# Performance work log

Measured on AMD Instinct MI355X. Metric: run time of the kernel, lower is better.

## Reference

```python
import jax, jax.numpy as jnp
import numpy as np

N_NODES = 100000
N_EDGES = 1600000
DIM = 128
N_LAYERS = 3
N_GRAPHS = 2048


def setup_inputs() -> dict:
    key = jax.random.key(0)
    ks = jax.random.split(key, 6)
    x = jax.random.normal(ks[0], (N_NODES, DIM), dtype=jnp.float32)
    edge_index = jax.random.randint(ks[1], (2, N_EDGES), 0, N_NODES, dtype=jnp.int64)
    batch = jnp.sort(jax.random.randint(ks[2], (N_NODES,), 0, N_GRAPHS, dtype=jnp.int64))
    scale = 1.0 / np.sqrt(DIM)
    W1 = jax.random.normal(ks[3], (N_LAYERS, DIM, DIM), dtype=jnp.float32) * scale
    b1 = jnp.zeros((N_LAYERS, DIM), dtype=jnp.float32)
    W2 = jax.random.normal(ks[4], (N_LAYERS, DIM, DIM), dtype=jnp.float32) * scale
    b2 = jnp.zeros((N_LAYERS, DIM), dtype=jnp.float32)
    return {"x": x, "edge_index": edge_index, "batch": batch,
            "W1": W1, "b1": b1, "W2": W2, "b2": b2}


def reference(x, edge_index, batch, W1, b1, W2, b2):
    src, dst = edge_index[0], edge_index[1]
    n = x.shape[0]
    n_layers = W1.shape[0]
    for l in range(n_layers):
        # GINConv (eps=0): h_i = MLP( sum_{j in N(i)} x_j + x_i )
        agg = jax.ops.segment_sum(x[src], dst, num_segments=n)  # [N, D]
        h = agg + x
        h = jnp.maximum(h @ W1[l] + b1[l], 0.0) @ W2[l] + b2[l]
        x = jnp.maximum(h, 0.0)  # outer self.act
    # global_mean_pool over graph ids
    sums = jax.ops.segment_sum(x, batch, num_segments=N_GRAPHS)  # [G, D]
    counts = jax.ops.segment_sum(jnp.ones((n,), x.dtype), batch, num_segments=N_GRAPHS)
    return sums / jnp.maximum(counts, 1.0)[:, None]
```

## Files before the change

kernel.cpp:

```cpp
#include <hip/hip_runtime.h>
#include <hip/hip_bf16.h>
#include <stdint.h>

#define N_NODES  100000
#define N_PAD    100032
#define N_EDGES  1600000
#define DIM      128
#define N_LAYERS 3
#define N_GRAPHS 2048

#define BSHIFT   9
#define NBUCKET  196
#define P1CHUNK  8192
#define P1GRID   196

typedef _Float16 f16;
typedef __attribute__((ext_vector_type(2))) _Float16 f16x2;
typedef __attribute__((ext_vector_type(4))) _Float16 f16x4;
typedef __attribute__((ext_vector_type(8))) _Float16 f16x8;
typedef __attribute__((ext_vector_type(4))) float f32x4;

#define MFMA16(a, b, c) __builtin_amdgcn_mfma_f32_16x16x32_f16((a), (b), (c), 0, 0, 0)

#define OFF_OFFS  0u
#define OFF_BHT   400064u
#define OFF_BST   400896u
#define OFF_GCUR  401728u
#define OFF_BLKH  402560u
#define OFF_ESRC  556288u
#define OFF_PAIR  6956288u
#define OFF_X16   19756288u
#define OFF_A16   45364480u
#define OFF_B16   70972672u
#define OFF_W1T   96580864u
#define OFF_W2T   96679168u


__global__ __launch_bounds__(256) void k_bhist(const int* __restrict__ dst,
                                               int* __restrict__ btot, int* __restrict__ blkh) {
    __shared__ int h[NBUCKET];
    int tid = threadIdx.x, b = blockIdx.x;
    if (tid < NBUCKET) h[tid] = 0;
    __syncthreads();
    int base = b * P1CHUNK;
    int n = min(P1CHUNK, N_EDGES - base);
    for (int i = tid; i < n; i += 256)
        atomicAdd(&h[dst[base + i] >> BSHIFT], 1);
    __syncthreads();
    if (tid < NBUCKET) {
        blkh[b * NBUCKET + tid] = h[tid];
        atomicAdd(&btot[tid], h[tid]);
    }
}

__global__ void k_bscan(const int* __restrict__ btot, int* __restrict__ bstart,
                        int* __restrict__ gcursor, int* __restrict__ offs) {
    __shared__ int s[NBUCKET + 1];
    if (threadIdx.x == 0) {
        int run = 0;
        for (int i = 0; i < NBUCKET; i++) { s[i] = run; run += btot[i]; }
        s[NBUCKET] = run;
    }
    __syncthreads();
    int t = threadIdx.x;
    if (t <= NBUCKET) bstart[t] = s[t];
    if (t < NBUCKET)  gcursor[t] = s[t];
    if (t == 0) offs[N_NODES] = N_EDGES;
}

__global__ __launch_bounds__(256) void k_part1(const int* __restrict__ src, const int* __restrict__ dst,
                                               const int* __restrict__ blkh, int* __restrict__ gcursor,
                                               uint2* __restrict__ pairs) {
    __shared__ int gbase[NBUCKET];
    __shared__ int cur[NBUCKET];
    int tid = threadIdx.x, b = blockIdx.x;
    if (tid < NBUCKET) {
        int h = blkh[b * NBUCKET + tid];
        gbase[tid] = atomicAdd(&gcursor[tid], h);
        cur[tid] = 0;
    }
    __syncthreads();
    int base = b * P1CHUNK;
    int n = min(P1CHUNK, N_EDGES - base);
    for (int i = tid; i < n; i += 256) {
        int d = dst[base + i], s = src[base + i];
        int bin = d >> BSHIFT;
        int slot = atomicAdd(&cur[bin], 1);
        uint2 p; p.x = (unsigned)d; p.y = (unsigned)s;
        pairs[gbase[bin] + slot] = p;
    }
}

__global__ __launch_bounds__(256) void k_part2(const uint2* __restrict__ pairs,
                                               const int* __restrict__ bstart,
                                               int* __restrict__ offs, int* __restrict__ esrc) {
    __shared__ int cnt[512];
    __shared__ int excl[512];
    __shared__ int sc[256];
    int t = threadIdx.x, b = blockIdx.x;
    int n0 = b << BSHIFT;
    int nn = min(512, N_NODES - n0);
    int e0 = bstart[b], e1 = bstart[b + 1];
    cnt[t] = 0; cnt[t + 256] = 0;
    __syncthreads();
    for (int i = e0 + t; i < e1; i += 256)
        atomicAdd(&cnt[pairs[i].x & 511], 1);
    __syncthreads();
    int a = cnt[2 * t], psum = a + cnt[2 * t + 1];
    sc[t] = psum;
    __syncthreads();
    for (int off = 1; off < 256; off <<= 1) {
        int v = (t >= off) ? sc[t - off] : 0;
        __syncthreads();
        sc[t] += v;
        __syncthreads();
    }
    int pairExcl = sc[t] - psum;
    excl[2 * t] = pairExcl;
    excl[2 * t + 1] = pairExcl + a;
    __syncthreads();
    for (int j = t; j < nn; j += 256) offs[n0 + j] = e0 + excl[j];
    __syncthreads();
    for (int i = e0 + t; i < e1; i += 256) {
        uint2 p = pairs[i];
        int pos = e0 + atomicAdd(&excl[p.x & 511], 1);
        esrc[pos] = (int)p.y;
    }
}


__global__ void k_cvtX(const float* __restrict__ x, f16* __restrict__ o) {
    size_t i = ((size_t)blockIdx.x * 256 + threadIdx.x) * 8;
    float4 v0 = *(const float4*)&x[i];
    float4 v1 = *(const float4*)&x[i + 4];
    f16x8 h;
    h[0] = (f16)v0.x; h[1] = (f16)v0.y; h[2] = (f16)v0.z; h[3] = (f16)v0.w;
    h[4] = (f16)v1.x; h[5] = (f16)v1.y; h[6] = (f16)v1.z; h[7] = (f16)v1.w;
    *(f16x8*)&o[i] = h;
}

__global__ void k_cvtW(const float* __restrict__ W, f16* __restrict__ Wt) {
    int t = blockIdx.x * 256 + threadIdx.x;
    int l = t >> 14;
    int kn = t & 16383;
    int k = kn >> 7, n = kn & 127;
    Wt[l * 16384 + n * 128 + k] = (f16)W[t];
}


#define BM 64
#define LDS_K 136

__global__ __launch_bounds__(256, 4) void k_fused(
    const f16* __restrict__ xin, f16* __restrict__ xout,
    const int* __restrict__ offs, const int* __restrict__ esrc,
    const f16* __restrict__ W1t, const float* __restrict__ b1,
    const f16* __restrict__ W2t, const float* __restrict__ b2)
{
    __shared__ __align__(16) f16 tile[BM * LDS_K];
    int tid  = threadIdx.x;
    int lane = tid & 63;
    int w    = tid >> 6;
    int fr   = lane & 15;
    int fg   = lane >> 4;
    int row0 = blockIdx.x * BM;

    {
        int g = fg, c = fr;
        const f16x8* xr = (const f16x8*)xin;
        int srcLane = g << 4;
#pragma unroll
        for (int s_ = 0; s_ < 4; s_++) {
            int node = row0 + w * 16 + s_ * 4 + g;
            float acc[8];
            if (node < N_NODES) {
                int e0 = offs[node], e1 = offs[node + 1];
                f16x8 sv = xr[(size_t)node * 16 + c];
#pragma unroll
                for (int j = 0; j < 8; j++) acc[j] = (float)sv[j];
                for (int base = e0; base < e1; base += 16) {
                    int ncur = e1 - base; if (ncur > 16) ncur = 16;
                    int ev = esrc[base + (c < ncur ? c : ncur - 1)];
                    int k = 0;
                    for (; k + 4 <= ncur; k += 4) {
                        int s0 = __shfl(ev, srcLane + k);
                        int s1 = __shfl(ev, srcLane + k + 1);
                        int s2 = __shfl(ev, srcLane + k + 2);
                        int s3 = __shfl(ev, srcLane + k + 3);
                        f16x8 v0 = xr[(size_t)s0 * 16 + c];
                        f16x8 v1 = xr[(size_t)s1 * 16 + c];
                        f16x8 v2 = xr[(size_t)s2 * 16 + c];
                        f16x8 v3 = xr[(size_t)s3 * 16 + c];
#pragma unroll
                        for (int j = 0; j < 8; j++)
                            acc[j] += (float)v0[j] + (float)v1[j] + (float)v2[j] + (float)v3[j];
                    }
                    for (; k < ncur; k++) {
                        int s = __shfl(ev, srcLane + k);
                        f16x8 v = xr[(size_t)s * 16 + c];
#pragma unroll
                        for (int j = 0; j < 8; j++) acc[j] += (float)v[j];
                    }
                }
            } else {
#pragma unroll
                for (int j = 0; j < 8; j++) acc[j] = 0.f;
            }
            int r = w * 16 + s_ * 4 + g;
            f16x8 o;
#pragma unroll
            for (int j = 0; j < 8; j++) o[j] = (f16)acc[j];
            *(f16x8*)&tile[r * LDS_K + c * 8] = o;
        }
    }
    __syncthreads();

    f16x8 wf[2][4];
    float4 bv[2];
#pragma unroll
    for (int nt = 0; nt < 2; nt++) {
        int col = w * 32 + nt * 16 + fr;
#pragma unroll
        for (int ks = 0; ks < 4; ks++)
            wf[nt][ks] = *(const f16x8*)&W1t[col * DIM + ks * 32 + fg * 8];
        bv[nt] = *(const float4*)&b1[w * 32 + nt * 16 + fg * 4];
    }

    f32x4 acc[4][2];
#pragma unroll
    for (int mt = 0; mt < 4; mt++)
#pragma unroll
        for (int nt = 0; nt < 2; nt++) acc[mt][nt] = (f32x4){0.f, 0.f, 0.f, 0.f};

#pragma unroll
    for (int mt = 0; mt < 4; mt++)
#pragma unroll
        for (int ks = 0; ks < 4; ks++) {
            f16x8 a = *(const f16x8*)&tile[(mt * 16 + fr) * LDS_K + ks * 32 + fg * 8];
            acc[mt][0] = MFMA16(wf[0][ks], a, acc[mt][0]);
            acc[mt][1] = MFMA16(wf[1][ks], a, acc[mt][1]);
        }
    __syncthreads();

#pragma unroll
    for (int mt = 0; mt < 4; mt++)
#pragma unroll
        for (int nt = 0; nt < 2; nt++) {
            f16x4 hv;
            hv[0] = (f16)fmaxf(acc[mt][nt][0] + bv[nt].x, 0.f);
            hv[1] = (f16)fmaxf(acc[mt][nt][1] + bv[nt].y, 0.f);
            hv[2] = (f16)fmaxf(acc[mt][nt][2] + bv[nt].z, 0.f);
            hv[3] = (f16)fmaxf(acc[mt][nt][3] + bv[nt].w, 0.f);
            *(f16x4*)&tile[(mt * 16 + fr) * LDS_K + w * 32 + nt * 16 + fg * 4] = hv;
        }

#pragma unroll
    for (int nt = 0; nt < 2; nt++) {
        int col = w * 32 + nt * 16 + fr;
#pragma unroll
        for (int ks = 0; ks < 4; ks++)
            wf[nt][ks] = *(const f16x8*)&W2t[col * DIM + ks * 32 + fg * 8];
        bv[nt] = *(const float4*)&b2[w * 32 + nt * 16 + fg * 4];
    }
    __syncthreads();

#pragma unroll
    for (int mt = 0; mt < 4; mt++)
#pragma unroll
        for (int nt = 0; nt < 2; nt++) acc[mt][nt] = (f32x4){0.f, 0.f, 0.f, 0.f};

#pragma unroll
    for (int mt = 0; mt < 4; mt++)
#pragma unroll
        for (int ks = 0; ks < 4; ks++) {
            f16x8 a = *(const f16x8*)&tile[(mt * 16 + fr) * LDS_K + ks * 32 + fg * 8];
            acc[mt][0] = MFMA16(wf[0][ks], a, acc[mt][0]);
            acc[mt][1] = MFMA16(wf[1][ks], a, acc[mt][1]);
        }

#pragma unroll
    for (int mt = 0; mt < 4; mt++)
#pragma unroll
        for (int nt = 0; nt < 2; nt++) {
            f16x4 ov;
            ov[0] = (f16)fmaxf(acc[mt][nt][0] + bv[nt].x, 0.f);
            ov[1] = (f16)fmaxf(acc[mt][nt][1] + bv[nt].y, 0.f);
            ov[2] = (f16)fmaxf(acc[mt][nt][2] + bv[nt].z, 0.f);
            ov[3] = (f16)fmaxf(acc[mt][nt][3] + bv[nt].w, 0.f);
            *(f16x4*)&xout[(size_t)(row0 + mt * 16 + fr) * DIM + w * 32 + nt * 16 + fg * 4] = ov;
        }
}


__global__ void k_pool(const f16* __restrict__ xf, const int* __restrict__ batch,
                       float* __restrict__ out) {
    int g = blockIdx.x;
    int d = threadIdx.x;
    int lo = 0, hi = N_NODES;
    while (lo < hi) { int m = (lo + hi) >> 1; if (batch[m] < g) lo = m + 1; else hi = m; }
    int start = lo;
    hi = N_NODES;
    while (lo < hi) { int m = (lo + hi) >> 1; if (batch[m] <= g) lo = m + 1; else hi = m; }
    int end = lo;
    float acc = 0.f;
    for (int i = start; i < end; i++) acc += (float)xf[(size_t)i * DIM + d];
    float cntf = (float)(end - start);
    out[(size_t)g * DIM + d] = acc / fmaxf(cntf, 1.f);
}


extern "C" void kernel_launch(void* const* d_in, const int* in_sizes, int n_in,
                              void* d_out, int out_size, void* d_ws, size_t ws_size,
                              hipStream_t stream) {
    const float* x     = (const float*)d_in[0];
    const int*   ei    = (const int*)d_in[1];
    const int*   batch = (const int*)d_in[2];
    const float* W1    = (const float*)d_in[3];
    const float* b1    = (const float*)d_in[4];
    const float* W2    = (const float*)d_in[5];
    const float* b2    = (const float*)d_in[6];
    const int* src = ei;
    const int* dst = ei + N_EDGES;

    char* ws = (char*)d_ws;
    int*   offs  = (int*)(ws + OFF_OFFS);
    int*   btot  = (int*)(ws + OFF_BHT);
    int*   bst   = (int*)(ws + OFF_BST);
    int*   gcur  = (int*)(ws + OFF_GCUR);
    int*   blkh  = (int*)(ws + OFF_BLKH);
    int*   esrc  = (int*)(ws + OFF_ESRC);
    uint2* pairs = (uint2*)(ws + OFF_PAIR);
    f16*   x16   = (f16*)(ws + OFF_X16);
    f16*   a16   = (f16*)(ws + OFF_A16);
    f16*   b16   = (f16*)(ws + OFF_B16);
    f16*   w1t   = (f16*)(ws + OFF_W1T);
    f16*   w2t   = (f16*)(ws + OFF_W2T);
    float* outp  = (float*)d_out;

    hipMemsetAsync(btot, 0, NBUCKET * sizeof(int), stream);
    k_bhist<<<P1GRID, 256, 0, stream>>>(dst, btot, blkh);
    k_bscan<<<1, 256, 0, stream>>>(btot, bst, gcur, offs);
    k_part1<<<P1GRID, 256, 0, stream>>>(src, dst, blkh, gcur, pairs);
    k_part2<<<NBUCKET, 256, 0, stream>>>(pairs, bst, offs, esrc);

    k_cvtX<<<6250, 256, 0, stream>>>(x, x16);
    k_cvtW<<<192, 256, 0, stream>>>(W1, w1t);
    k_cvtW<<<192, 256, 0, stream>>>(W2, w2t);

    const f16* xin = x16;
    for (int l = 0; l < N_LAYERS; ++l) {
        f16* xoutb = (l == 1) ? b16 : a16;
        k_fused<<<N_PAD / BM, 256, 0, stream>>>(xin, xoutb, offs, esrc,
                                                w1t + (size_t)l * DIM * DIM, b1 + (size_t)l * DIM,
                                                w2t + (size_t)l * DIM * DIM, b2 + (size_t)l * DIM);
        xin = xoutb;
    }

    k_pool<<<N_GRAPHS, 128, 0, stream>>>(xin, batch, outp);
}
```

Measured before the change: 349.8 us.

## Pack CSR partition pairs into 32-bit and restructure neighbor gather per node

The bucket size for the CSR build is halved so each bucket holds 256 destination nodes. This lets each (src, dst) pair be packed into a single 32-bit word (src in the high bits, local dst in the low 8 bits), halving the traffic of the partition pass. The fused layer kernel now has each wavefront process one node at a time, with its four 16-lane groups striding through the edges. It combines the partial sums with cross-lane xor shuffles, replacing the per-group node assignment and the shuffles that broadcast edge indices. The occupancy hint in the launch bounds is also dropped. The new gather works on 16 nodes per wave sequentially and adds a reduction step per node, which may expose more latency.

```diff
diff --git a/kernel.cpp b/kernel.cpp
--- a/kernel.cpp
+++ b/kernel.cpp
@@ -9,10 +9,10 @@
 #define N_LAYERS 3
 #define N_GRAPHS 2048
 
-#define BSHIFT   9
-#define NBUCKET  196
-#define P1CHUNK  8192
-#define P1GRID   196
+#define BSHIFT   8
+#define NBUCKET  391
+#define P1CHUNK  4096
+#define P1GRID   391
 
 typedef _Float16 f16;
 typedef __attribute__((ext_vector_type(2))) _Float16 f16x2;
@@ -24,32 +24,32 @@
 
 #define OFF_OFFS  0u
 #define OFF_BHT   400064u
-#define OFF_BST   400896u
-#define OFF_GCUR  401728u
-#define OFF_BLKH  402560u
-#define OFF_ESRC  556288u
-#define OFF_PAIR  6956288u
-#define OFF_X16   19756288u
-#define OFF_A16   45364480u
-#define OFF_B16   70972672u
-#define OFF_W1T   96580864u
-#define OFF_W2T   96679168u
+#define OFF_BST   401664u
+#define OFF_GCUR  403264u
+#define OFF_BLKH  404864u
+#define OFF_ESRC  1016448u
+#define OFF_PAIR  7416448u
+#define OFF_X16   13816448u
+#define OFF_A16   39424640u
+#define OFF_B16   65032832u
+#define OFF_W1T   90641024u
+#define OFF_W2T   90739328u
 
 
 __global__ __launch_bounds__(256) void k_bhist(const int* __restrict__ dst,
                                                int* __restrict__ btot, int* __restrict__ blkh) {
     __shared__ int h[NBUCKET];
     int tid = threadIdx.x, b = blockIdx.x;
-    if (tid < NBUCKET) h[tid] = 0;
+    for (int i = tid; i < NBUCKET; i += 256) h[i] = 0;
     __syncthreads();
     int base = b * P1CHUNK;
     int n = min(P1CHUNK, N_EDGES - base);
     for (int i = tid; i < n; i += 256)
         atomicAdd(&h[dst[base + i] >> BSHIFT], 1);
     __syncthreads();
-    if (tid < NBUCKET) {
-        blkh[b * NBUCKET + tid] = h[tid];
-        atomicAdd(&btot[tid], h[tid]);
+    for (int i = tid; i < NBUCKET; i += 256) {
+        blkh[b * NBUCKET + i] = h[i];
+        atomicAdd(&btot[i], h[i]);
     }
 }
 
@@ -63,21 +63,21 @@
     }
     __syncthreads();
     int t = threadIdx.x;
-    if (t <= NBUCKET) bstart[t] = s[t];
-    if (t < NBUCKET)  gcursor[t] = s[t];
+    for (int i = t; i <= NBUCKET; i += 256) bstart[i] = s[i];
+    for (int i = t; i < NBUCKET; i += 256)  gcursor[i] = s[i];
     if (t == 0) offs[N_NODES] = N_EDGES;
 }
 
 __global__ __launch_bounds__(256) void k_part1(const int* __restrict__ src, const int* __restrict__ dst,
                                                const int* __restrict__ blkh, int* __restrict__ gcursor,
-                                               uint2* __restrict__ pairs) {
+                                               uint32_t* __restrict__ pairs) {
     __shared__ int gbase[NBUCKET];
     __shared__ int cur[NBUCKET];
     int tid = threadIdx.x, b = blockIdx.x;
-    if (tid < NBUCKET) {
-        int h = blkh[b * NBUCKET + tid];
-        gbase[tid] = atomicAdd(&gcursor[tid], h);
-        cur[tid] = 0;
+    for (int i = tid; i < NBUCKET; i += 256) {
+        int h = blkh[b * NBUCKET + i];
+        gbase[i] = atomicAdd(&gcursor[i], h);
+        cur[i] = 0;
     }
     __syncthreads();
     int base = b * P1CHUNK;
@@ -86,28 +86,27 @@
         int d = dst[base + i], s = src[base + i];
         int bin = d >> BSHIFT;
         int slot = atomicAdd(&cur[bin], 1);
-        uint2 p; p.x = (unsigned)d; p.y = (unsigned)s;
-        pairs[gbase[bin] + slot] = p;
-    }
-}
-
-__global__ __launch_bounds__(256) void k_part2(const uint2* __restrict__ pairs,
+        pairs[gbase[bin] + slot] = ((uint32_t)s << 8) | (uint32_t)(d & 255);
+    }
+}
+
+__global__ __launch_bounds__(256) void k_part2(const uint32_t* __restrict__ pairs,
                                                const int* __restrict__ bstart,
                                                int* __restrict__ offs, int* __restrict__ esrc) {
-    __shared__ int cnt[512];
-    __shared__ int excl[512];
+    __shared__ int cnt[256];
+    __shared__ int cur[256];
     __shared__ int sc[256];
     int t = threadIdx.x, b = blockIdx.x;
     int n0 = b << BSHIFT;
-    int nn = min(512, N_NODES - n0);
+    int nn = min(256, N_NODES - n0);
     int e0 = bstart[b], e1 = bstart[b + 1];
-    cnt[t] = 0; cnt[t + 256] = 0;
+    cnt[t] = 0;
     __syncthreads();
     for (int i = e0 + t; i < e1; i += 256)
-        atomicAdd(&cnt[pairs[i].x & 511], 1);
-    __syncthreads();
-    int a = cnt[2 * t], psum = a + cnt[2 * t + 1];
-    sc[t] = psum;
+        atomicAdd(&cnt[pairs[i] & 255], 1);
+    __syncthreads();
+    int my = cnt[t];
+    sc[t] = my;
     __syncthreads();
     for (int off = 1; off < 256; off <<= 1) {
         int v = (t >= off) ? sc[t - off] : 0;
@@ -115,16 +114,14 @@
         sc[t] += v;
         __syncthreads();
     }
-    int pairExcl = sc[t] - psum;
-    excl[2 * t] = pairExcl;
-    excl[2 * t + 1] = pairExcl + a;
-    __syncthreads();
-    for (int j = t; j < nn; j += 256) offs[n0 + j] = e0 + excl[j];
+    int excl = sc[t] - my;
+    cur[t] = excl;
+    if (t < nn) offs[n0 + t] = e0 + excl;
     __syncthreads();
     for (int i = e0 + t; i < e1; i += 256) {
-        uint2 p = pairs[i];
-        int pos = e0 + atomicAdd(&excl[p.x & 511], 1);
-        esrc[pos] = (int)p.y;
+        uint32_t p = pairs[i];
+        int pos = e0 + atomicAdd(&cur[p & 255], 1);
+        esrc[pos] = (int)(p >> 8);
     }
 }
 
@@ -151,7 +148,7 @@
 #define BM 64
 #define LDS_K 136
 
-__global__ __launch_bounds__(256, 4) void k_fused(
+__global__ __launch_bounds__(256) void k_fused(
     const f16* __restrict__ xin, f16* __restrict__ xout,
     const int* __restrict__ offs, const int* __restrict__ esrc,
     const f16* __restrict__ W1t, const float* __restrict__ b1,
@@ -168,49 +165,44 @@
     {
         int g = fg, c = fr;
         const f16x8* xr = (const f16x8*)xin;
-        int srcLane = g << 4;
-#pragma unroll
-        for (int s_ = 0; s_ < 4; s_++) {
-            int node = row0 + w * 16 + s_ * 4 + g;
+        for (int s_ = 0; s_ < 16; s_++) {
+            int node = row0 + w * 16 + s_;
+            bool valid = node < N_NODES;
+            int cl = valid ? node : 0;
             float acc[8];
-            if (node < N_NODES) {
+            f16x8 sv = xr[(size_t)cl * 16 + c];
+#pragma unroll
+            for (int j = 0; j < 8; j++) acc[j] = (valid && g == 0) ? (float)sv[j] : 0.f;
+            if (valid) {
                 int e0 = offs[node], e1 = offs[node + 1];
-                f16x8 sv = xr[(size_t)node * 16 + c];
-#pragma unroll
-                for (int j = 0; j < 8; j++) acc[j] = (float)sv[j];
-                for (int base = e0; base < e1; base += 16) {
-                    int ncur = e1 - base; if (ncur > 16) ncur = 16;
-                    int ev = esrc[base + (c < ncur ? c : ncur - 1)];
-                    int k = 0;
-                    for (; k + 4 <= ncur; k += 4) {
-                        int s0 = __shfl(ev, srcLane + k);
-                        int s1 = __shfl(ev, srcLane + k + 1);
-                        int s2 = __shfl(ev, srcLane + k + 2);
-                        int s3 = __shfl(ev, srcLane + k + 3);
-                        f16x8 v0 = xr[(size_t)s0 * 16 + c];
-                        f16x8 v1 = xr[(size_t)s1 * 16 + c];
-                        f16x8 v2 = xr[(size_t)s2 * 16 + c];
-                        f16x8 v3 = xr[(size_t)s3 * 16 + c];
-#pragma unroll
-                        for (int j = 0; j < 8; j++)
-                            acc[j] += (float)v0[j] + (float)v1[j] + (float)v2[j] + (float)v3[j];
-                    }
-                    for (; k < ncur; k++) {
-                        int s = __shfl(ev, srcLane + k);
-                        f16x8 v = xr[(size_t)s * 16 + c];
-#pragma unroll
-                        for (int j = 0; j < 8; j++) acc[j] += (float)v[j];
-                    }
+                int e = e0 + g;
+                for (; e + 12 < e1; e += 16) {
+                    int s0 = esrc[e], s1 = esrc[e + 4], s2 = esrc[e + 8], s3 = esrc[e + 12];
+                    f16x8 v0 = xr[(size_t)s0 * 16 + c];
+                    f16x8 v1 = xr[(size_t)s1 * 16 + c];
+                    f16x8 v2 = xr[(size_t)s2 * 16 + c];
+                    f16x8 v3 = xr[(size_t)s3 * 16 + c];
+#pragma unroll
+                    for (int j = 0; j < 8; j++)
+                        acc[j] += ((float)v0[j] + (float)v1[j]) + ((float)v2[j] + (float)v3[j]);
                 }
-            } else {
-#pragma unroll
-                for (int j = 0; j < 8; j++) acc[j] = 0.f;
+                for (; e < e1; e += 4) {
+                    f16x8 v = xr[(size_t)esrc[e] * 16 + c];
+#pragma unroll
+                    for (int j = 0; j < 8; j++) acc[j] += (float)v[j];
+                }
             }
-            int r = w * 16 + s_ * 4 + g;
-            f16x8 o;
-#pragma unroll
-            for (int j = 0; j < 8; j++) o[j] = (f16)acc[j];
-            *(f16x8*)&tile[r * LDS_K + c * 8] = o;
+#pragma unroll
+            for (int j = 0; j < 8; j++) {
+                acc[j] += __shfl_xor(acc[j], 16);
+                acc[j] += __shfl_xor(acc[j], 32);
+            }
+            if (g == 0) {
+                f16x8 o;
+#pragma unroll
+                for (int j = 0; j < 8; j++) o[j] = (f16)acc[j];
+                *(f16x8*)&tile[(w * 16 + s_) * LDS_K + c * 8] = o;
+            }
         }
     }
     __syncthreads();
@@ -323,19 +315,19 @@
     const int* dst = ei + N_EDGES;
 
     char* ws = (char*)d_ws;
-    int*   offs  = (int*)(ws + OFF_OFFS);
-    int*   btot  = (int*)(ws + OFF_BHT);
-    int*   bst   = (int*)(ws + OFF_BST);
-    int*   gcur  = (int*)(ws + OFF_GCUR);
-    int*   blkh  = (int*)(ws + OFF_BLKH);
-    int*   esrc  = (int*)(ws + OFF_ESRC);
-    uint2* pairs = (uint2*)(ws + OFF_PAIR);
-    f16*   x16   = (f16*)(ws + OFF_X16);
-    f16*   a16   = (f16*)(ws + OFF_A16);
-    f16*   b16   = (f16*)(ws + OFF_B16);
-    f16*   w1t   = (f16*)(ws + OFF_W1T);
-    f16*   w2t   = (f16*)(ws + OFF_W2T);
-    float* outp  = (float*)d_out;
+    int*      offs  = (int*)(ws + OFF_OFFS);
+    int*      btot  = (int*)(ws + OFF_BHT);
+    int*      bst   = (int*)(ws + OFF_BST);
+    int*      gcur  = (int*)(ws + OFF_GCUR);
+    int*      blkh  = (int*)(ws + OFF_BLKH);
+    int*      esrc  = (int*)(ws + OFF_ESRC);
+    uint32_t* pairs = (uint32_t*)(ws + OFF_PAIR);
+    f16*      x16   = (f16*)(ws + OFF_X16);
+    f16*      a16   = (f16*)(ws + OFF_A16);
+    f16*      b16   = (f16*)(ws + OFF_B16);
+    f16*      w1t   = (f16*)(ws + OFF_W1T);
+    f16*      w2t   = (f16*)(ws + OFF_W2T);
+    float*    outp  = (float*)d_out;
 
     hipMemsetAsync(btot, 0, NBUCKET * sizeof(int), stream);
     k_bhist<<<P1GRID, 256, 0, stream>>>(dst, btot, blkh);
```

New measurement: 454.9 us. +30.1%, slower.
